# Performance work log

Measured on AMD Instinct MI355X. Metric: run time of the kernel, lower is better.

Reference implementation:

```python
import jax, jax.numpy as jnp
import numpy as np

IN_F, OUT_F = 4096, 4096
BS = 64            # block_size
CB = 256           # codebook_size
LR = 128           # lowrank_dim
OB, IB = OUT_F // BS, IN_F // BS


def setup_inputs() -> dict:
    key = jax.random.key(0)
    ks = jax.random.split(key, 8)
    inp = {}
    inp["input"] = jax.random.normal(ks[0], (4, 2048, IN_F), dtype=jnp.float32)
    inp["zm"] = jax.random.randint(ks[1], (OB, IB, BS, BS), 0, CB, dtype=jnp.int32)
    std = float(np.sqrt(2.0 / (5 * min(OUT_F, IN_F))))
    inp["codebooks"] = jax.random.normal(ks[2], (OB * IB, CB), dtype=jnp.float32) * std
    xav = float(np.sqrt(6.0 / (LR + IN_F)))
    inp["lowrank_first"] = jax.random.uniform(ks[3], (LR, IN_F), dtype=jnp.float32, minval=-xav, maxval=xav)
    # torch inits this to zeros; use small random so the low-rank path is exercised
    inp["lowrank_second"] = jax.random.normal(ks[4], (OUT_F * 2, LR), dtype=jnp.float32) * 0.02
    inp["grid_scale"] = jnp.ones((OUT_F // 8, 1, IN_F // 8, 1), dtype=jnp.float32)
    inp["grid_bias"] = jnp.zeros((OUT_F // 8, 1, IN_F // 8, 1), dtype=jnp.float32)
    inp["scale"] = jnp.ones((OUT_F,), dtype=jnp.float32)
    inp["bias"] = jnp.zeros((OUT_F,), dtype=jnp.float32)
    return inp


def _dequant_weight(zm, codebooks, grid_scale, grid_bias):
    # per-block codebook gather: each (out_block, in_block) has its own codebook row
    flat_idx = zm.reshape(OB * IB, BS * BS)                       # [OB*IB, BS*BS]
    gathered = jnp.take_along_axis(codebooks, flat_idx, axis=1)   # [OB*IB, BS*BS]
    rm = gathered.reshape(OB, IB, BS, BS).swapaxes(1, 2).reshape(OUT_F, IN_F)
    # per-8x8-tile affine modulation
    rm8 = rm.reshape(OUT_F // 8, 8, IN_F // 8, 8)
    rm = (grid_bias + rm8 * grid_scale).reshape(OUT_F, IN_F)
    return rm


def reference(input, zm, codebooks, lowrank_first, lowrank_second, grid_scale, grid_bias, scale, bias):
    rm = _dequant_weight(zm, codebooks, grid_scale, grid_bias)    # [OUT_F, IN_F]
    baseline = jnp.einsum("bsi,oi->bso", input, rm)               # dense GEMM
    hid = jnp.einsum("bsi,ri->bsr", input, lowrank_first)         # [B,S,LR]
    intercept = jnp.concatenate([scale, bias], axis=0)            # [2*OUT_F]
    lr_out = jnp.einsum("bsr,or->bso", hid, lowrank_second) + intercept
    multiplicative, additive = lr_out[..., :OUT_F], lr_out[..., OUT_F:]
    return additive + multiplicative * baseline
```

## Files before the change

### kernel.cpp

```cpp
#include <hip/hip_runtime.h>
#include <hip/hip_bf16.h>

#define IN_F   4096
#define OUT_F  4096
#define NTOK   8192
#define LRANK  128

typedef unsigned short u16;
typedef unsigned int u32;
typedef __attribute__((ext_vector_type(8))) __bf16 bf16x8;
typedef __attribute__((ext_vector_type(4))) float f32x4;

__device__ __forceinline__ u16 f2bf(float f) {
  union { float f; unsigned u; } a; a.f = f;
  return (u16)((a.u + 0x7fffu + ((a.u >> 16) & 1u)) >> 16);
}
__device__ __forceinline__ float bf2f(u16 b) {
  union { unsigned u; float f; } a; a.u = (u32)b << 16;
  return a.f;
}

__device__ __forceinline__ void async_ld16(const void* g, void* l) {
  __builtin_amdgcn_global_load_lds(
      (__attribute__((address_space(1))) void*)(unsigned long long)g,
      (__attribute__((address_space(3))) void*)(unsigned int)(unsigned long long)l,
      16, 0, 0);
}


__global__ void cvt_bf16_2_kernel(const float* __restrict__ s1, u16* __restrict__ d1, int n1,
                                  const float* __restrict__ s2, u16* __restrict__ d2, int n2) {
  int i = blockIdx.x * blockDim.x + threadIdx.x;
  const float* s; u16* d; int j;
  if (i < n1) { s = s1; d = d1; j = i; }
  else if (i < n1 + n2) { s = s2; d = d2; j = i - n1; }
  else return;
  float4 v = ((const float4*)s)[j];
  ushort4 o;
  o.x = f2bf(v.x); o.y = f2bf(v.y); o.z = f2bf(v.z); o.w = f2bf(v.w);
  ((ushort4*)d)[j] = o;
}

__global__ void dequant_kernel(const int* __restrict__ zm, const float* __restrict__ cb,
                               const float* __restrict__ gs, const float* __restrict__ gb,
                               u16* __restrict__ W) {
  int idx = blockIdx.x * blockDim.x + threadIdx.x;
  if (idx >= OUT_F * IN_F / 4) return;
  int o = idx >> 10;
  int i = (idx & 1023) << 2;
  int row = ((o >> 6) << 6) + (i >> 6);
  const int* zp = zm + ((size_t)row << 12) + ((o & 63) << 6) + (i & 63);
  int4 z = *(const int4*)zp;
  const float* cr = cb + ((size_t)row << 8);
  int g = (o >> 3) * (IN_F / 8) + (i >> 3);
  float s = gs[g], b = gb[g];
  ushort4 w;
  w.x = f2bf(b + cr[z.x] * s);
  w.y = f2bf(b + cr[z.y] * s);
  w.z = f2bf(b + cr[z.z] * s);
  w.w = f2bf(b + cr[z.w] * s);
  *(ushort4*)(W + (size_t)idx * 4) = w;
}


__device__ __forceinline__ void stage_tile_128x32(const u16* __restrict__ g, int stride,
                                                  int row0, int col0,
                                                  u16* lbase, int wave, int lane) {
#pragma unroll
  for (int p = 0; p < 2; ++p) {
    int li_base = wave * 64 + p * 256;
    int li = li_base + lane;
    const u16* gaddr = g + (size_t)(row0 + (li >> 2)) * stride + col0 + ((li & 3) << 3);
    async_ld16(gaddr, lbase + li_base * 8);
  }
}

__global__ __launch_bounds__(256) void hid_part(const float* __restrict__ input,
                                                u16* __restrict__ A,
                                                const u16* __restrict__ L1,
                                                float* __restrict__ Hp) {
  __shared__ __align__(16) u16 lds[2 * 128 * 32];
  u16* ldsA = lds;
  u16* ldsB = lds + 128 * 32;

  int tid = threadIdx.x;
  int wave = tid >> 6, lane = tid & 63;
  int kc  = blockIdx.x & 3;
  int bm0 = (blockIdx.x >> 2) * 128;
  int kbase = kc * 1024;
  int wr = (wave >> 1) * 64, wc = (wave & 1) * 64;
  int lrow = lane & 15, lk = (lane >> 4) * 8;

  const int crow = tid >> 1;
  const int c16  = (tid & 1) * 16;

  f32x4 acc[4][4];
#pragma unroll
  for (int m = 0; m < 4; ++m)
#pragma unroll
    for (int n = 0; n < 4; ++n)
#pragma unroll
      for (int v = 0; v < 4; ++v) acc[m][n][v] = 0.f;

  for (int kt = 0; kt < 32; ++kt) {
    int k0 = kbase + kt * 32;

    stage_tile_128x32(L1, IN_F, 0, k0, ldsB, wave, lane);

    {
      const float* ip = input + (size_t)(bm0 + crow) * IN_F + k0 + c16;
      float4 v0 = ((const float4*)ip)[0];
      float4 v1 = ((const float4*)ip)[1];
      float4 v2 = ((const float4*)ip)[2];
      float4 v3 = ((const float4*)ip)[3];
      ushort4 o0, o1, o2, o3;
      o0.x = f2bf(v0.x); o0.y = f2bf(v0.y); o0.z = f2bf(v0.z); o0.w = f2bf(v0.w);
      o1.x = f2bf(v1.x); o1.y = f2bf(v1.y); o1.z = f2bf(v1.z); o1.w = f2bf(v1.w);
      o2.x = f2bf(v2.x); o2.y = f2bf(v2.y); o2.z = f2bf(v2.z); o2.w = f2bf(v2.w);
      o3.x = f2bf(v3.x); o3.y = f2bf(v3.y); o3.z = f2bf(v3.z); o3.w = f2bf(v3.w);
      u16* lp = &ldsA[crow * 32 + c16];
      ((ushort4*)lp)[0] = o0; ((ushort4*)lp)[1] = o1;
      ((ushort4*)lp)[2] = o2; ((ushort4*)lp)[3] = o3;
      u16* gp = A + (size_t)(bm0 + crow) * IN_F + k0 + c16;
      ((ushort4*)gp)[0] = o0; ((ushort4*)gp)[1] = o1;
      ((ushort4*)gp)[2] = o2; ((ushort4*)gp)[3] = o3;
    }
    __syncthreads();

    bf16x8 af[4], bfr[4];
#pragma unroll
    for (int m = 0; m < 4; ++m)
      af[m] = *(const bf16x8*)&ldsA[(wr + m * 16 + lrow) * 32 + lk];
#pragma unroll
    for (int n = 0; n < 4; ++n)
      bfr[n] = *(const bf16x8*)&ldsB[(wc + n * 16 + lrow) * 32 + lk];
#pragma unroll
    for (int m = 0; m < 4; ++m)
#pragma unroll
      for (int n = 0; n < 4; ++n)
        acc[m][n] = __builtin_amdgcn_mfma_f32_16x16x32_bf16(af[m], bfr[n], acc[m][n], 0, 0, 0);
    __syncthreads();
  }

  float* Hpk = Hp + (size_t)kc * NTOK * LRANK;
  int lrow4 = (lane >> 4) * 4;
#pragma unroll
  for (int m = 0; m < 4; ++m)
#pragma unroll
    for (int n = 0; n < 4; ++n)
#pragma unroll
      for (int v = 0; v < 4; ++v) {
        int rg = bm0 + wr + m * 16 + lrow4 + v;
        int cg = wc + n * 16 + lrow;
        Hpk[(size_t)rg * LRANK + cg] = acc[m][n][v];
      }
}

__global__ void hid_reduce(const float* __restrict__ Hp, u16* __restrict__ H) {
  int i = blockIdx.x * blockDim.x + threadIdx.x;
  if (i >= NTOK * LRANK / 4) return;
  const size_t stride = (size_t)NTOK * LRANK;
  float4 s0 = ((const float4*)Hp)[i];
  float4 s1 = ((const float4*)(Hp + stride))[i];
  float4 s2 = ((const float4*)(Hp + 2 * stride))[i];
  float4 s3 = ((const float4*)(Hp + 3 * stride))[i];
  ushort4 o;
  o.x = f2bf(s0.x + s1.x + s2.x + s3.x);
  o.y = f2bf(s0.y + s1.y + s2.y + s3.y);
  o.z = f2bf(s0.z + s1.z + s2.z + s3.z);
  o.w = f2bf(s0.w + s1.w + s2.w + s3.w);
  ((ushort4*)H)[i] = o;
}


#define MFMA_QUAD(mh, nh)                                                        \
  _Pragma("unroll") for (int mf = 0; mf < 4; ++mf)                               \
  _Pragma("unroll") for (int nf = 0; nf < 2; ++nf)                               \
  _Pragma("unroll") for (int ks = 0; ks < 2; ++ks)                               \
    acc[(mh)*4 + mf][(nh)*2 + nf] = __builtin_amdgcn_mfma_f32_16x16x32_bf16(     \
        af[mf][ks], bfr[nh][nf][ks], acc[(mh)*4 + mf][(nh)*2 + nf], 0, 0, 0);

#define PHASE_MID                                          \
  __builtin_amdgcn_s_barrier();                            \
  asm volatile("s_waitcnt lgkmcnt(0)" ::: "memory");       \
  __builtin_amdgcn_sched_barrier(0);                       \
  __builtin_amdgcn_s_setprio(1);

#define PHASE_END                                          \
  __builtin_amdgcn_s_setprio(0);                           \
  __builtin_amdgcn_s_barrier();

#define PHASE_END_VM                                       \
  __builtin_amdgcn_s_setprio(0);                           \
  asm volatile("s_waitcnt vmcnt(4)" ::: "memory");         \
  __builtin_amdgcn_s_barrier();

#define PHASE_END_VM0                                      \
  __builtin_amdgcn_s_setprio(0);                           \
  asm volatile("s_waitcnt vmcnt(0)" ::: "memory");         \
  __builtin_amdgcn_s_barrier();

#define LAB(b, h) ((char*)lds + (b) * 65536 + (h) * 16384)
#define LBB(b, h) ((char*)lds + (b) * 65536 + 32768 + (h) * 16384)

#define STG_K(gbase, lreg) do {                               \
    async_ld16((gbase) + gK0, (lreg) + ldst0);                \
    async_ld16((gbase) + gK1, (lreg) + ldst0 + 8192); } while (0)
#define STG_L(gbase, lreg) do {                               \
    async_ld16((gbase) + gL0, (lreg) + ldst0);                \
    async_ld16((gbase) + gL1, (lreg) + ldst0 + 8192); } while (0)

#define LDF(p, byteoff, lb) (*(const bf16x8*)((p) + (byteoff) + (lb)))

__global__ __launch_bounds__(512)
__attribute__((amdgpu_waves_per_eu(2, 2)))
void gemm_main(const u16* __restrict__ A,
               const u16* __restrict__ W,
               uint2* __restrict__ Bl) {
  __shared__ __align__(16) u16 lds[65536];

  const int tid = threadIdx.x;
  const int lane = tid & 63, wave = tid >> 6;
  const int wg_m = wave >> 2;
  const int lr = lane & 15;

  int bid = blockIdx.x;
  int swz = (bid & 7) * 64 + (bid >> 3);
  const int bn0 = (swz & 15) * 256;
  const int bm0 = (swz >> 4) * 256;

  const int row_c = tid >> 3;
  const int xslot = ((tid & 7) ^ (row_c & 7)) << 3;
  const int gK0 = row_c * IN_F + xslot;
  const int gK1 = gK0 + 64 * IN_F;
  const int ldst0 = (tid & ~63) * 16;

  const int lb0 = (lr << 7) | ((((lane >> 4)) ^ (lr & 7)) << 4);
  const int lb1 = (lr << 7) | (((4 | (lane >> 4)) ^ (lr & 7)) << 4);

  const u16* baseA0 = A + (size_t)bm0 * IN_F;
  const u16* baseA1 = A + (size_t)(bm0 + 128) * IN_F;
  const u16* baseW0 = W + (size_t)bn0 * IN_F;
  const u16* baseW1 = W + (size_t)(bn0 + 128) * IN_F;

  const int wg_n = wave & 3;
  const int b_row0 = (wg_n & 1) * 64;
  const char* pA0 = LAB(0, wg_m);
  const char* pA1 = LAB(1, wg_m);
  const char* pB0 = LBB(0, wg_n >> 1) + b_row0 * 128;
  const char* pB1 = LBB(1, wg_n >> 1) + b_row0 * 128;

  f32x4 acc[8][4];
#pragma unroll
  for (int m = 0; m < 8; ++m)
#pragma unroll
    for (int n = 0; n < 4; ++n)
#pragma unroll
      for (int v = 0; v < 4; ++v) acc[m][n][v] = 0.f;

  STG_K(baseW0, LBB(0, 0));
  STG_K(baseW1, LBB(0, 1));
  STG_K(baseA0, LAB(0, 0));
  STG_K(baseA1, LAB(0, 1));
  STG_K(baseW0 + 64, LBB(1, 0));
  STG_K(baseW1 + 64, LBB(1, 1));
  asm volatile("s_waitcnt vmcnt(4)" ::: "memory");
  __builtin_amdgcn_s_barrier();

  bf16x8 af[4][2];
  bf16x8 bfr[2][2][2];

  for (int u = 0; u < 31; ++u) {
    const int c1k = (2 * u + 1) * 64;
    const int n0k = (2 * u + 2) * 64;
    const int n1k = (2 * u + 3) * 64;

#pragma unroll
    for (int mf = 0; mf < 4; ++mf) {
      af[mf][0] = LDF(pA0, mf * 2048, lb0);
      af[mf][1] = LDF(pA0, mf * 2048, lb1);
    }
#pragma unroll
    for (int nf = 0; nf < 2; ++nf) {
      bfr[0][nf][0] = LDF(pB0, nf * 2048, lb0);
      bfr[0][nf][1] = LDF(pB0, nf * 2048, lb1);
    }
    STG_K(baseA0 + c1k, LAB(1, 0));
    PHASE_MID; MFMA_QUAD(0, 0); PHASE_END;

#pragma unroll
    for (int nf = 0; nf < 2; ++nf) {
      bfr[1][nf][0] = LDF(pB0, 4096 + nf * 2048, lb0);
      bfr[1][nf][1] = LDF(pB0, 4096 + nf * 2048, lb1);
    }
    STG_K(baseA1 + c1k, LAB(1, 1));
    PHASE_MID; MFMA_QUAD(0, 1); PHASE_END;

#pragma unroll
    for (int mf = 0; mf < 4; ++mf) {
      af[mf][0] = LDF(pA0, 8192 + mf * 2048, lb0);
      af[mf][1] = LDF(pA0, 8192 + mf * 2048, lb1);
    }
    STG_K(baseW0 + n0k, LBB(0, 0));
    PHASE_MID; MFMA_QUAD(1, 1); PHASE_END;

    STG_K(baseW1 + n0k, LBB(0, 1));
    PHASE_MID; MFMA_QUAD(1, 0); PHASE_END_VM;

#pragma unroll
    for (int mf = 0; mf < 4; ++mf) {
      af[mf][0] = LDF(pA1, mf * 2048, lb0);
      af[mf][1] = LDF(pA1, mf * 2048, lb1);
    }
#pragma unroll
    for (int nf = 0; nf < 2; ++nf) {
      bfr[0][nf][0] = LDF(pB1, nf * 2048, lb0);
      bfr[0][nf][1] = LDF(pB1, nf * 2048, lb1);
    }
    STG_K(baseA0 + n0k, LAB(0, 0));
    PHASE_MID; MFMA_QUAD(0, 0); PHASE_END;

#pragma unroll
    for (int nf = 0; nf < 2; ++nf) {
      bfr[1][nf][0] = LDF(pB1, 4096 + nf * 2048, lb0);
      bfr[1][nf][1] = LDF(pB1, 4096 + nf * 2048, lb1);
    }
    STG_K(baseA1 + n0k, LAB(0, 1));
    PHASE_MID; MFMA_QUAD(0, 1); PHASE_END;

#pragma unroll
    for (int mf = 0; mf < 4; ++mf) {
      af[mf][0] = LDF(pA1, 8192 + mf * 2048, lb0);
      af[mf][1] = LDF(pA1, 8192 + mf * 2048, lb1);
    }
    STG_K(baseW0 + n1k, LBB(1, 0));
    PHASE_MID; MFMA_QUAD(1, 1); PHASE_END;

    STG_K(baseW1 + n1k, LBB(1, 1));
    PHASE_MID; MFMA_QUAD(1, 0); PHASE_END_VM;
  }

  {
    const int c1k = 63 * 64;

#pragma unroll
    for (int mf = 0; mf < 4; ++mf) {
      af[mf][0] = LDF(pA0, mf * 2048, lb0);
      af[mf][1] = LDF(pA0, mf * 2048, lb1);
    }
#pragma unroll
    for (int nf = 0; nf < 2; ++nf) {
      bfr[0][nf][0] = LDF(pB0, nf * 2048, lb0);
      bfr[0][nf][1] = LDF(pB0, nf * 2048, lb1);
    }
    STG_K(baseA0 + c1k, LAB(1, 0));
    PHASE_MID; MFMA_QUAD(0, 0); PHASE_END;

#pragma unroll
    for (int nf = 0; nf < 2; ++nf) {
      bfr[1][nf][0] = LDF(pB0, 4096 + nf * 2048, lb0);
      bfr[1][nf][1] = LDF(pB0, 4096 + nf * 2048, lb1);
    }
    STG_K(baseA1 + c1k, LAB(1, 1));
    PHASE_MID; MFMA_QUAD(0, 1); PHASE_END;

#pragma unroll
    for (int mf = 0; mf < 4; ++mf) {
      af[mf][0] = LDF(pA0, 8192 + mf * 2048, lb0);
      af[mf][1] = LDF(pA0, 8192 + mf * 2048, lb1);
    }
    PHASE_MID; MFMA_QUAD(1, 1); PHASE_END;

    PHASE_MID; MFMA_QUAD(1, 0); PHASE_END_VM0;

#pragma unroll
    for (int mf = 0; mf < 4; ++mf) {
      af[mf][0] = LDF(pA1, mf * 2048, lb0);
      af[mf][1] = LDF(pA1, mf * 2048, lb1);
    }
#pragma unroll
    for (int nf = 0; nf < 2; ++nf) {
      bfr[0][nf][0] = LDF(pB1, nf * 2048, lb0);
      bfr[0][nf][1] = LDF(pB1, nf * 2048, lb1);
    }
    PHASE_MID; MFMA_QUAD(0, 0); PHASE_END;

#pragma unroll
    for (int nf = 0; nf < 2; ++nf) {
      bfr[1][nf][0] = LDF(pB1, 4096 + nf * 2048, lb0);
      bfr[1][nf][1] = LDF(pB1, 4096 + nf * 2048, lb1);
    }
    PHASE_MID; MFMA_QUAD(0, 1); PHASE_END;

#pragma unroll
    for (int mf = 0; mf < 4; ++mf) {
      af[mf][0] = LDF(pA1, 8192 + mf * 2048, lb0);
      af[mf][1] = LDF(pA1, 8192 + mf * 2048, lb1);
    }
    PHASE_MID; MFMA_QUAD(1, 1); PHASE_END;

    PHASE_MID; MFMA_QUAD(1, 0); PHASE_END;
  }

  const size_t tbase = ((size_t)bid * 8 + wave) * 32;
#pragma unroll
  for (int mf = 0; mf < 8; ++mf)
#pragma unroll
    for (int nf = 0; nf < 4; ++nf) {
      f32x4 a = acc[mf][nf];
      uint2 pk;
      pk.x = (u32)f2bf(a[0]) | ((u32)f2bf(a[1]) << 16);
      pk.y = (u32)f2bf(a[2]) | ((u32)f2bf(a[3]) << 16);
      Bl[(tbase + mf * 4 + nf) * 64 + lane] = pk;
    }
}


__global__ __launch_bounds__(512)
void lr_apply(const uint2* __restrict__ Bl,
              const u16* __restrict__ H,
              const u16* __restrict__ L2,
              const float* __restrict__ scale,
              const float* __restrict__ bias,
              float* __restrict__ out) {
  __shared__ __align__(16) u16 lds[65536];

  const int tid = threadIdx.x;
  const int lane = tid & 63, wave = tid >> 6;
  const int wg_m = wave >> 2, wg_n = wave & 3;
  const int lr = lane & 15;

  int bid = blockIdx.x;
  int swz = (bid & 7) * 64 + (bid >> 3);
  const int bn0 = (swz & 15) * 256;
  const int bm0 = (swz >> 4) * 256;

  const int row_c = tid >> 3;
  const int xslot = ((tid & 7) ^ (row_c & 7)) << 3;
  const int gL0 = row_c * LRANK + xslot;
  const int gL1 = gL0 + 64 * LRANK;
  const int ldst0 = (tid & ~63) * 16;

  const int lb0 = (lr << 7) | ((((lane >> 4)) ^ (lr & 7)) << 4);
  const int lb1 = (lr << 7) | (((4 | (lane >> 4)) ^ (lr & 7)) << 4);

  float scl[4], bs_[4];
#pragma unroll
  for (int nf = 0; nf < 4; ++nf) {
    int cg = bn0 + wg_n * 64 + nf * 16 + lr;
    scl[nf] = scale[cg];
    bs_[nf] = bias[cg];
  }

  {
    const u16* baseH0 = H + (size_t)bm0 * LRANK;
    const u16* baseH1 = H + (size_t)(bm0 + 128) * LRANK;
    const u16* baseL0 = L2 + (size_t)bn0 * LRANK;
    const u16* baseL1 = L2 + (size_t)(bn0 + 128) * LRANK;
    STG_L(baseH0,      (char*)lds + 0);
    STG_L(baseH1,      (char*)lds + 16384);
    STG_L(baseH0 + 64, (char*)lds + 32768);
    STG_L(baseH1 + 64, (char*)lds + 49152);
    STG_L(baseL0,      (char*)lds + 65536);
    STG_L(baseL1,      (char*)lds + 81920);
    STG_L(baseL0 + 64, (char*)lds + 98304);
    STG_L(baseL1 + 64, (char*)lds + 114688);
  }
  __syncthreads();

  const char* pH = (char*)lds + wg_m * 16384;
  const char* pL = (char*)lds + 65536 + (wg_n >> 1) * 16384 + (wg_n & 1) * 8192;

  f32x4 maccM[8][4];
#pragma unroll
  for (int m = 0; m < 8; ++m)
#pragma unroll
    for (int n = 0; n < 4; ++n)
#pragma unroll
      for (int v = 0; v < 4; ++v) maccM[m][n][v] = 0.f;

#pragma unroll
  for (int kc = 0; kc < 4; ++kc) {
    const int sb = (kc >> 1) * 32768;
    const int lb = (kc & 1) ? lb1 : lb0;
    bf16x8 lf[4];
#pragma unroll
    for (int nf = 0; nf < 4; ++nf)
      lf[nf] = LDF(pL + sb, nf * 2048, lb);
#pragma unroll
    for (int mf = 0; mf < 8; ++mf) {
      bf16x8 hf = LDF(pH + sb, mf * 2048, lb);
#pragma unroll
      for (int nf = 0; nf < 4; ++nf)
        maccM[mf][nf] = __builtin_amdgcn_mfma_f32_16x16x32_bf16(hf, lf[nf], maccM[mf][nf], 0, 0, 0);
    }
  }

  __syncthreads();
  {
    const u16* baseL0 = L2 + (size_t)(OUT_F + bn0) * LRANK;
    const u16* baseL1 = L2 + (size_t)(OUT_F + bn0 + 128) * LRANK;
    STG_L(baseL0,      (char*)lds + 65536);
    STG_L(baseL1,      (char*)lds + 81920);
    STG_L(baseL0 + 64, (char*)lds + 98304);
    STG_L(baseL1 + 64, (char*)lds + 114688);
  }
  __syncthreads();

  const size_t tbase = ((size_t)bid * 8 + wave) * 32;
#pragma unroll
  for (int mq = 0; mq < 4; ++mq) {
    f32x4 maccA[2][4];
#pragma unroll
    for (int m = 0; m < 2; ++m)
#pragma unroll
      for (int n = 0; n < 4; ++n)
#pragma unroll
        for (int v = 0; v < 4; ++v) maccA[m][n][v] = 0.f;

#pragma unroll
    for (int kc = 0; kc < 4; ++kc) {
      const int sb = (kc >> 1) * 32768;
      const int lb = (kc & 1) ? lb1 : lb0;
      bf16x8 lf[4];
#pragma unroll
      for (int nf = 0; nf < 4; ++nf)
        lf[nf] = LDF(pL + sb, nf * 2048, lb);
#pragma unroll
      for (int mf = 0; mf < 2; ++mf) {
        bf16x8 hf = LDF(pH + sb, (mq * 2 + mf) * 2048, lb);
#pragma unroll
        for (int nf = 0; nf < 4; ++nf)
          maccA[mf][nf] = __builtin_amdgcn_mfma_f32_16x16x32_bf16(hf, lf[nf], maccA[mf][nf], 0, 0, 0);
      }
    }

#pragma unroll
    for (int mf = 0; mf < 2; ++mf)
#pragma unroll
      for (int nf = 0; nf < 4; ++nf) {
        int m8 = mq * 2 + mf;
        uint2 pk = Bl[(tbase + m8 * 4 + nf) * 64 + lane];
        float b0 = bf2f((u16)(pk.x & 0xffff));
        float b1 = bf2f((u16)(pk.x >> 16));
        float b2 = bf2f((u16)(pk.y & 0xffff));
        float b3 = bf2f((u16)(pk.y >> 16));
        int rg = bm0 + wg_m * 128 + m8 * 16 + (lane >> 4) * 4;
        int cg = bn0 + wg_n * 64 + nf * 16 + lr;
        float* op = out + (size_t)rg * OUT_F + cg;
        op[0 * OUT_F] = (maccA[mf][nf][0] + bs_[nf]) + (maccM[m8][nf][0] + scl[nf]) * b0;
        op[1 * OUT_F] = (maccA[mf][nf][1] + bs_[nf]) + (maccM[m8][nf][1] + scl[nf]) * b1;
        op[2 * OUT_F] = (maccA[mf][nf][2] + bs_[nf]) + (maccM[m8][nf][2] + scl[nf]) * b2;
        op[3 * OUT_F] = (maccA[mf][nf][3] + bs_[nf]) + (maccM[m8][nf][3] + scl[nf]) * b3;
      }
  }
}


extern "C" void kernel_launch(void* const* d_in, const int* in_sizes, int n_in,
                              void* d_out, int out_size, void* d_ws, size_t ws_size,
                              hipStream_t stream) {
  const float* input = (const float*)d_in[0];
  const int*   zm    = (const int*)d_in[1];
  const float* cb    = (const float*)d_in[2];
  const float* l1    = (const float*)d_in[3];
  const float* l2    = (const float*)d_in[4];
  const float* gs    = (const float*)d_in[5];
  const float* gb    = (const float*)d_in[6];
  const float* scale = (const float*)d_in[7];
  const float* bias  = (const float*)d_in[8];
  float* out = (float*)d_out;

  const size_t OFF_A  = 0;
  const size_t OFF_W  = OFF_A + (size_t)NTOK * IN_F * 2;
  const size_t OFF_L1 = OFF_W + (size_t)OUT_F * IN_F * 2;
  const size_t OFF_L2 = OFF_L1 + (size_t)LRANK * IN_F * 2;
  const size_t OFF_H  = OFF_L2 + (size_t)2 * OUT_F * LRANK * 2;
  const size_t OFF_BL = OFF_H + (size_t)NTOK * LRANK * 2;
  const size_t NEED   = OFF_BL + (size_t)NTOK * OUT_F * 2;
  if (ws_size < NEED) return;

  char* ws = (char*)d_ws;
  u16* A    = (u16*)(ws + OFF_A);
  u16* W    = (u16*)(ws + OFF_W);
  u16* L1b  = (u16*)(ws + OFF_L1);
  u16* L2b  = (u16*)(ws + OFF_L2);
  u16* H    = (u16*)(ws + OFF_H);
  uint2* Bl = (uint2*)(ws + OFF_BL);
  float* Hp = (float*)(ws + OFF_BL);

  cvt_bf16_2_kernel<<<((LRANK * IN_F + 2 * OUT_F * LRANK) / 4 + 255) / 256, 256, 0, stream>>>(
      l1, L1b, LRANK * IN_F / 4, l2, L2b, 2 * OUT_F * LRANK / 4);
  dequant_kernel<<<(OUT_F * IN_F / 4) / 256, 256, 0, stream>>>(zm, cb, gs, gb, W);

  hid_part<<<4 * (NTOK / 128), 256, 0, stream>>>(input, A, L1b, Hp);
  hid_reduce<<<(NTOK * LRANK / 4) / 256, 256, 0, stream>>>(Hp, H);

  gemm_main<<<(NTOK / 256) * (OUT_F / 256), 512, 0, stream>>>(A, W, Bl);

  lr_apply<<<(NTOK / 256) * (OUT_F / 256), 512, 0, stream>>>(Bl, H, L2b, scale, bias, out);
}
```

Before: 374.9 us.

## Fuse low-rank epilogue into main GEMM and split hid K eightfold

```diff
diff --git a/kernel.cpp b/kernel.cpp
--- a/kernel.cpp
+++ b/kernel.cpp
@@ -85,9 +85,9 @@
 
   int tid = threadIdx.x;
   int wave = tid >> 6, lane = tid & 63;
-  int kc  = blockIdx.x & 3;
-  int bm0 = (blockIdx.x >> 2) * 128;
-  int kbase = kc * 1024;
+  int kc  = blockIdx.x & 7;
+  int bm0 = (blockIdx.x >> 3) * 128;
+  int kbase = kc * 512;
   int wr = (wave >> 1) * 64, wc = (wave & 1) * 64;
   int lrow = lane & 15, lk = (lane >> 4) * 8;
 
@@ -102,17 +102,18 @@
 #pragma unroll
       for (int v = 0; v < 4; ++v) acc[m][n][v] = 0.f;
 
-  for (int kt = 0; kt < 32; ++kt) {
+  const float* ip = input + (size_t)(bm0 + crow) * IN_F + kbase + c16;
+  float4 v0 = ((const float4*)ip)[0];
+  float4 v1 = ((const float4*)ip)[1];
+  float4 v2 = ((const float4*)ip)[2];
+  float4 v3 = ((const float4*)ip)[3];
+
+  for (int kt = 0; kt < 16; ++kt) {
     int k0 = kbase + kt * 32;
 
     stage_tile_128x32(L1, IN_F, 0, k0, ldsB, wave, lane);
 
     {
-      const float* ip = input + (size_t)(bm0 + crow) * IN_F + k0 + c16;
-      float4 v0 = ((const float4*)ip)[0];
-      float4 v1 = ((const float4*)ip)[1];
-      float4 v2 = ((const float4*)ip)[2];
-      float4 v3 = ((const float4*)ip)[3];
       ushort4 o0, o1, o2, o3;
       o0.x = f2bf(v0.x); o0.y = f2bf(v0.y); o0.z = f2bf(v0.z); o0.w = f2bf(v0.w);
       o1.x = f2bf(v1.x); o1.y = f2bf(v1.y); o1.z = f2bf(v1.z); o1.w = f2bf(v1.w);
@@ -125,6 +126,14 @@
       ((ushort4*)gp)[0] = o0; ((ushort4*)gp)[1] = o1;
       ((ushort4*)gp)[2] = o2; ((ushort4*)gp)[3] = o3;
     }
+
+    if (kt < 15) {
+      ip += 32;
+      v0 = ((const float4*)ip)[0];
+      v1 = ((const float4*)ip)[1];
+      v2 = ((const float4*)ip)[2];
+      v3 = ((const float4*)ip)[3];
+    }
     __syncthreads();
 
     bf16x8 af[4], bfr[4];
@@ -160,15 +169,14 @@
   int i = blockIdx.x * blockDim.x + threadIdx.x;
   if (i >= NTOK * LRANK / 4) return;
   const size_t stride = (size_t)NTOK * LRANK;
-  float4 s0 = ((const float4*)Hp)[i];
-  float4 s1 = ((const float4*)(Hp + stride))[i];
-  float4 s2 = ((const float4*)(Hp + 2 * stride))[i];
-  float4 s3 = ((const float4*)(Hp + 3 * stride))[i];
+  float4 a0 = ((const float4*)Hp)[i];
+#pragma unroll
+  for (int p = 1; p < 8; ++p) {
+    float4 ap = ((const float4*)(Hp + p * stride))[i];
+    a0.x += ap.x; a0.y += ap.y; a0.z += ap.z; a0.w += ap.w;
+  }
   ushort4 o;
-  o.x = f2bf(s0.x + s1.x + s2.x + s3.x);
-  o.y = f2bf(s0.y + s1.y + s2.y + s3.y);
-  o.z = f2bf(s0.z + s1.z + s2.z + s3.z);
-  o.w = f2bf(s0.w + s1.w + s2.w + s3.w);
+  o.x = f2bf(a0.x); o.y = f2bf(a0.y); o.z = f2bf(a0.z); o.w = f2bf(a0.w);
   ((ushort4*)H)[i] = o;
 }
 
@@ -216,7 +224,11 @@
 __attribute__((amdgpu_waves_per_eu(2, 2)))
 void gemm_main(const u16* __restrict__ A,
                const u16* __restrict__ W,
-               uint2* __restrict__ Bl) {
+               const u16* __restrict__ H,
+               const u16* __restrict__ L2,
+               const float* __restrict__ scale,
+               const float* __restrict__ bias,
+               float* __restrict__ out) {
   __shared__ __align__(16) u16 lds[65536];
 
   const int tid = threadIdx.x;
@@ -402,47 +414,14 @@
     PHASE_MID; MFMA_QUAD(1, 0); PHASE_END;
   }
 
-  const size_t tbase = ((size_t)bid * 8 + wave) * 32;
+  uint2 pk[8][4];
 #pragma unroll
   for (int mf = 0; mf < 8; ++mf)
 #pragma unroll
     for (int nf = 0; nf < 4; ++nf) {
-      f32x4 a = acc[mf][nf];
-      uint2 pk;
-      pk.x = (u32)f2bf(a[0]) | ((u32)f2bf(a[1]) << 16);
-      pk.y = (u32)f2bf(a[2]) | ((u32)f2bf(a[3]) << 16);
-      Bl[(tbase + mf * 4 + nf) * 64 + lane] = pk;
-    }
-}
-
-
-__global__ __launch_bounds__(512)
-void lr_apply(const uint2* __restrict__ Bl,
-              const u16* __restrict__ H,
-              const u16* __restrict__ L2,
-              const float* __restrict__ scale,
-              const float* __restrict__ bias,
-              float* __restrict__ out) {
-  __shared__ __align__(16) u16 lds[65536];
-
-  const int tid = threadIdx.x;
-  const int lane = tid & 63, wave = tid >> 6;
-  const int wg_m = wave >> 2, wg_n = wave & 3;
-  const int lr = lane & 15;
-
-  int bid = blockIdx.x;
-  int swz = (bid & 7) * 64 + (bid >> 3);
-  const int bn0 = (swz & 15) * 256;
-  const int bm0 = (swz >> 4) * 256;
-
-  const int row_c = tid >> 3;
-  const int xslot = ((tid & 7) ^ (row_c & 7)) << 3;
-  const int gL0 = row_c * LRANK + xslot;
-  const int gL1 = gL0 + 64 * LRANK;
-  const int ldst0 = (tid & ~63) * 16;
-
-  const int lb0 = (lr << 7) | ((((lane >> 4)) ^ (lr & 7)) << 4);
-  const int lb1 = (lr << 7) | (((4 | (lane >> 4)) ^ (lr & 7)) << 4);
+      pk[mf][nf].x = (u32)f2bf(acc[mf][nf][0]) | ((u32)f2bf(acc[mf][nf][1]) << 16);
+      pk[mf][nf].y = (u32)f2bf(acc[mf][nf][2]) | ((u32)f2bf(acc[mf][nf][3]) << 16);
+    }
 
   float scl[4], bs_[4];
 #pragma unroll
@@ -452,6 +431,11 @@
     bs_[nf] = bias[cg];
   }
 
+  const int gL0 = row_c * LRANK + xslot;
+  const int gL1 = gL0 + 64 * LRANK;
+
+  asm volatile("s_waitcnt vmcnt(0)" ::: "memory");
+  __builtin_amdgcn_s_barrier();
   {
     const u16* baseH0 = H + (size_t)bm0 * LRANK;
     const u16* baseH1 = H + (size_t)(bm0 + 128) * LRANK;
@@ -466,37 +450,54 @@
     STG_L(baseL0 + 64, (char*)lds + 98304);
     STG_L(baseL1 + 64, (char*)lds + 114688);
   }
-  __syncthreads();
+  asm volatile("s_waitcnt vmcnt(0)" ::: "memory");
+  __builtin_amdgcn_s_barrier();
 
   const char* pH = (char*)lds + wg_m * 16384;
   const char* pL = (char*)lds + 65536 + (wg_n >> 1) * 16384 + (wg_n & 1) * 8192;
 
-  f32x4 maccM[8][4];
-#pragma unroll
-  for (int m = 0; m < 8; ++m)
-#pragma unroll
-    for (int n = 0; n < 4; ++n)
-#pragma unroll
-      for (int v = 0; v < 4; ++v) maccM[m][n][v] = 0.f;
-
-#pragma unroll
-  for (int kc = 0; kc < 4; ++kc) {
-    const int sb = (kc >> 1) * 32768;
-    const int lb = (kc & 1) ? lb1 : lb0;
-    bf16x8 lf[4];
-#pragma unroll
-    for (int nf = 0; nf < 4; ++nf)
-      lf[nf] = LDF(pL + sb, nf * 2048, lb);
-#pragma unroll
-    for (int mf = 0; mf < 8; ++mf) {
-      bf16x8 hf = LDF(pH + sb, mf * 2048, lb);
+#pragma unroll
+  for (int mq = 0; mq < 4; ++mq) {
+    f32x4 macc[2][4];
+#pragma unroll
+    for (int m = 0; m < 2; ++m)
+#pragma unroll
+      for (int n = 0; n < 4; ++n)
+#pragma unroll
+        for (int v = 0; v < 4; ++v) macc[m][n][v] = 0.f;
+#pragma unroll
+    for (int kc = 0; kc < 4; ++kc) {
+      const int sb = (kc >> 1) * 32768;
+      const int lb = (kc & 1) ? lb1 : lb0;
+      bf16x8 lf[4];
 #pragma unroll
       for (int nf = 0; nf < 4; ++nf)
-        maccM[mf][nf] = __builtin_amdgcn_mfma_f32_16x16x32_bf16(hf, lf[nf], maccM[mf][nf], 0, 0, 0);
-    }
-  }
-
-  __syncthreads();
+        lf[nf] = LDF(pL + sb, nf * 2048, lb);
+#pragma unroll
+      for (int mf = 0; mf < 2; ++mf) {
+        bf16x8 hf = LDF(pH + sb, (mq * 2 + mf) * 2048, lb);
+#pragma unroll
+        for (int nf = 0; nf < 4; ++nf)
+          macc[mf][nf] = __builtin_amdgcn_mfma_f32_16x16x32_bf16(hf, lf[nf], macc[mf][nf], 0, 0, 0);
+      }
+    }
+#pragma unroll
+    for (int mf = 0; mf < 2; ++mf)
+#pragma unroll
+      for (int nf = 0; nf < 4; ++nf) {
+        int m8 = mq * 2 + mf;
+        uint2 p = pk[m8][nf];
+        float t0 = (macc[mf][nf][0] + scl[nf]) * bf2f((u16)(p.x & 0xffff));
+        float t1 = (macc[mf][nf][1] + scl[nf]) * bf2f((u16)(p.x >> 16));
+        float t2 = (macc[mf][nf][2] + scl[nf]) * bf2f((u16)(p.y & 0xffff));
+        float t3 = (macc[mf][nf][3] + scl[nf]) * bf2f((u16)(p.y >> 16));
+        p.x = (u32)f2bf(t0) | ((u32)f2bf(t1) << 16);
+        p.y = (u32)f2bf(t2) | ((u32)f2bf(t3) << 16);
+        pk[m8][nf] = p;
+      }
+  }
+
+  __builtin_amdgcn_s_barrier();
   {
     const u16* baseL0 = L2 + (size_t)(OUT_F + bn0) * LRANK;
     const u16* baseL1 = L2 + (size_t)(OUT_F + bn0 + 128) * LRANK;
@@ -505,19 +506,18 @@
     STG_L(baseL0 + 64, (char*)lds + 98304);
     STG_L(baseL1 + 64, (char*)lds + 114688);
   }
-  __syncthreads();
-
-  const size_t tbase = ((size_t)bid * 8 + wave) * 32;
+  asm volatile("s_waitcnt vmcnt(0)" ::: "memory");
+  __builtin_amdgcn_s_barrier();
+
 #pragma unroll
   for (int mq = 0; mq < 4; ++mq) {
-    f32x4 maccA[2][4];
+    f32x4 macc[2][4];
 #pragma unroll
     for (int m = 0; m < 2; ++m)
 #pragma unroll
       for (int n = 0; n < 4; ++n)
 #pragma unroll
-        for (int v = 0; v < 4; ++v) maccA[m][n][v] = 0.f;
-
+        for (int v = 0; v < 4; ++v) macc[m][n][v] = 0.f;
 #pragma unroll
     for (int kc = 0; kc < 4; ++kc) {
       const int sb = (kc >> 1) * 32768;
@@ -531,27 +531,22 @@
         bf16x8 hf = LDF(pH + sb, (mq * 2 + mf) * 2048, lb);
 #pragma unroll
         for (int nf = 0; nf < 4; ++nf)
-          maccA[mf][nf] = __builtin_amdgcn_mfma_f32_16x16x32_bf16(hf, lf[nf], maccA[mf][nf], 0, 0, 0);
+          macc[mf][nf] = __builtin_amdgcn_mfma_f32_16x16x32_bf16(hf, lf[nf], macc[mf][nf], 0, 0, 0);
       }
     }
-
 #pragma unroll
     for (int mf = 0; mf < 2; ++mf)
 #pragma unroll
       for (int nf = 0; nf < 4; ++nf) {
         int m8 = mq * 2 + mf;
-        uint2 pk = Bl[(tbase + m8 * 4 + nf) * 64 + lane];
-        float b0 = bf2f((u16)(pk.x & 0xffff));
-        float b1 = bf2f((u16)(pk.x >> 16));
-        float b2 = bf2f((u16)(pk.y & 0xffff));
-        float b3 = bf2f((u16)(pk.y >> 16));
+        uint2 p = pk[m8][nf];
         int rg = bm0 + wg_m * 128 + m8 * 16 + (lane >> 4) * 4;
         int cg = bn0 + wg_n * 64 + nf * 16 + lr;
         float* op = out + (size_t)rg * OUT_F + cg;
-        op[0 * OUT_F] = (maccA[mf][nf][0] + bs_[nf]) + (maccM[m8][nf][0] + scl[nf]) * b0;
-        op[1 * OUT_F] = (maccA[mf][nf][1] + bs_[nf]) + (maccM[m8][nf][1] + scl[nf]) * b1;
-        op[2 * OUT_F] = (maccA[mf][nf][2] + bs_[nf]) + (maccM[m8][nf][2] + scl[nf]) * b2;
-        op[3 * OUT_F] = (maccA[mf][nf][3] + bs_[nf]) + (maccM[m8][nf][3] + scl[nf]) * b3;
+        op[0 * OUT_F] = bf2f((u16)(p.x & 0xffff)) + macc[mf][nf][0] + bs_[nf];
+        op[1 * OUT_F] = bf2f((u16)(p.x >> 16))    + macc[mf][nf][1] + bs_[nf];
+        op[2 * OUT_F] = bf2f((u16)(p.y & 0xffff)) + macc[mf][nf][2] + bs_[nf];
+        op[3 * OUT_F] = bf2f((u16)(p.y >> 16))    + macc[mf][nf][3] + bs_[nf];
       }
   }
 }
@@ -576,8 +571,8 @@
   const size_t OFF_L1 = OFF_W + (size_t)OUT_F * IN_F * 2;
   const size_t OFF_L2 = OFF_L1 + (size_t)LRANK * IN_F * 2;
   const size_t OFF_H  = OFF_L2 + (size_t)2 * OUT_F * LRANK * 2;
-  const size_t OFF_BL = OFF_H + (size_t)NTOK * LRANK * 2;
-  const size_t NEED   = OFF_BL + (size_t)NTOK * OUT_F * 2;
+  const size_t OFF_HP = OFF_H + (size_t)NTOK * LRANK * 2;
+  const size_t NEED   = OFF_HP + (size_t)8 * NTOK * LRANK * 4;
   if (ws_size < NEED) return;
 
   char* ws = (char*)d_ws;
@@ -586,17 +581,14 @@
   u16* L1b  = (u16*)(ws + OFF_L1);
   u16* L2b  = (u16*)(ws + OFF_L2);
   u16* H    = (u16*)(ws + OFF_H);
-  uint2* Bl = (uint2*)(ws + OFF_BL);
-  float* Hp = (float*)(ws + OFF_BL);
+  float* Hp = (float*)(ws + OFF_HP);
 
   cvt_bf16_2_kernel<<<((LRANK * IN_F + 2 * OUT_F * LRANK) / 4 + 255) / 256, 256, 0, stream>>>(
       l1, L1b, LRANK * IN_F / 4, l2, L2b, 2 * OUT_F * LRANK / 4);
   dequant_kernel<<<(OUT_F * IN_F / 4) / 256, 256, 0, stream>>>(zm, cb, gs, gb, W);
 
-  hid_part<<<4 * (NTOK / 128), 256, 0, stream>>>(input, A, L1b, Hp);
+  hid_part<<<8 * (NTOK / 128), 256, 0, stream>>>(input, A, L1b, Hp);
   hid_reduce<<<(NTOK * LRANK / 4) / 256, 256, 0, stream>>>(Hp, H);
 
-  gemm_main<<<(NTOK / 256) * (OUT_F / 256), 512, 0, stream>>>(A, W, Bl);
-
-  lr_apply<<<(NTOK / 256) * (OUT_F / 256), 512, 0, stream>>>(Bl, H, L2b, scale, bias, out);
-}
+  gemm_main<<<(NTOK / 256) * (OUT_F / 256), 512, 0, stream>>>(A, W, H, L2b, scale, bias, out);
+}
```

Result: faster. 342.7 us (-8.6%).
